# Kernel optimization log

Measured on AMD Instinct MI355X. Metric: run time of the kernel, lower is better.

## Reference

```python
import jax, jax.numpy as jnp
import numpy as np

B, L, H, D = 4096, 256, 32, 2
LOG_PROB_FACTOR = 0.5

def setup_inputs() -> dict:
    key = jax.random.key(0)
    k0, k1, k2, k3 = jax.random.split(key, 4)
    x = jax.random.randint(k0, (B, L), 0, D)  # spin configs in {0,1}
    Wi = jax.random.normal(k1, (D, 4 * H), dtype=jnp.float32) * 0.1   # input kernel (no bias, flax LSTMCell)
    Wh = jax.random.normal(k2, (H, 4 * H), dtype=jnp.float32) * 0.1   # recurrent kernel
    bh = jnp.zeros((4 * H,), dtype=jnp.float32)                        # recurrent bias
    Wo = jax.random.normal(k3, (H, D), dtype=jnp.float32) * 0.1       # output Dense kernel
    bo = jnp.zeros((D,), dtype=jnp.float32)                            # output Dense bias
    return {"x": x, "Wi": Wi, "Wh": Wh, "bh": bh, "Wo": Wo, "bo": bo}

def reference(x, Wi, Wh, bh, Wo, bo):
    # one-hot of spin t-1 (zeros at t=0); log-prob is read out at spin t.
    x_oh = jax.nn.one_hot(x, D, dtype=Wi.dtype)      # [B, L, D]
    xs = jnp.swapaxes(x_oh, 0, 1)                    # [L, B, D] time-major for scan
    c0 = jnp.zeros((x.shape[0], H), Wi.dtype)
    h0 = jnp.zeros((x.shape[0], H), Wi.dtype)
    inp0 = jnp.zeros((x.shape[0], D), Wi.dtype)      # jnp.zeros(inputDim) initial input

    def step(carry, xt):
        c, h, inp = carry
        gates = inp @ Wi + h @ Wh + bh               # [B, 4H]
        i, f, g, o = jnp.split(gates, 4, axis=-1)    # flax LSTMCell gate order i,f,g,o
        c_new = jax.nn.sigmoid(f) * c + jax.nn.sigmoid(i) * jnp.tanh(g)
        h_new = jax.nn.sigmoid(o) * jnp.tanh(c_new)
        out = jax.nn.elu(h_new @ Wo + bo)            # Dense + actFun, [B, D]
        # log(sum(softmax(out) * onehot)) == gathered log_softmax (stable form)
        logp = jnp.sum(jax.nn.log_softmax(out, axis=-1) * xt, axis=-1)  # [B]
        return (c_new, h_new, xt), logp

    _, logps = jax.lax.scan(step, (c0, h0, inp0), xs)  # logps: [L, B]
    return LOG_PROB_FACTOR * jnp.sum(logps, axis=0)    # [B]
```

## Files before the change

### kernel.cpp

```cpp
#include <hip/hip_runtime.h>


typedef __attribute__((ext_vector_type(8))) short bf16x8;
typedef __attribute__((ext_vector_type(4))) float f32x4;

#define LOG2E  1.4426950408889634f
#define TWOL   2.8853900817779268f
#define LN2    0.6931471805599453f

__device__ __forceinline__ float fexp2(float x) { return __builtin_amdgcn_exp2f(x); }
__device__ __forceinline__ float flog2(float x) { return __builtin_amdgcn_logf(x); }
__device__ __forceinline__ float frcp(float x)  { return __builtin_amdgcn_rcpf(x); }

__device__ __forceinline__ float fsig(float x)   { return frcp(1.f + fexp2(-LOG2E * x)); }
__device__ __forceinline__ float ftanh_(float x) { return 1.f - 2.f * frcp(fexp2(TWOL * x) + 1.f); }
__device__ __forceinline__ float felu(float x)   { return x > 0.f ? x : fexp2(LOG2E * x) - 1.f; }

__device__ __forceinline__ unsigned short f2bf(float f) {
    unsigned u = __builtin_bit_cast(unsigned, f);
    u = (u + 0x7FFFu + ((u >> 16) & 1u)) >> 16;
    return (unsigned short)u;
}

constexpr int Bsz = 4096;

__global__ __launch_bounds__(512, 2) void lstm_r11(
    const int*   __restrict__ x,
    const float* __restrict__ Wi,
    const float* __restrict__ Wh,
    const float* __restrict__ bh,
    const float* __restrict__ Wo,
    const float* __restrict__ bo,
    float*       __restrict__ out)
{
    const int tid  = threadIdx.x;
    const int w    = tid >> 6;
    const int lane = tid & 63;
    const int m    = lane & 15;
    const int oct  = lane >> 4;
    const int rot  = w & 3;
    const int half = w >> 2;
    const int b0   = blockIdx.x * 16;

    __shared__ unsigned spinbits[16][8];
    __shared__ float2   Sbuf[256][16];
    __shared__ short    hbuf[2][16][40];
    __shared__ float    red[8][16];

    {
        const int bl = tid >> 5;
        const int c8 = (tid & 31) * 8;
        const int4* src = reinterpret_cast<const int4*>(x + (b0 + bl) * 256 + c8);
        const int4 v0 = src[0], v1 = src[1];
        const unsigned bv =
            (v0.x & 1) | ((v0.y & 1) << 1) | ((v0.z & 1) << 2) | ((v0.w & 1) << 3) |
            ((v1.x & 1) << 4) | ((v1.y & 1) << 5) | ((v1.z & 1) << 6) | ((v1.w & 1) << 7);
        reinterpret_cast<char*>(spinbits)[bl * 32 + (tid & 31)] = (char)bv;
    }

    bf16x8 wfrag[4];
#pragma unroll
    for (int q = 0; q < 4; ++q) {
        const float gs = (q == 2) ? TWOL * 0.5f * 2.f : -LOG2E;
        const float gss = (q == 2) ? TWOL : -LOG2E;
        (void)gs;
        const int colg = 32 * q + 16 * half + ((m + rot) & 15);
#pragma unroll
        for (int j = 0; j < 8; ++j)
            wfrag[q][j] = (short)f2bf(((q == 2) ? TWOL * 0.5f : -LOG2E) * 2.f * 0.5f * Wh[(oct * 8 + j) * 128 + colg] * ((q == 2) ? 2.f : 1.f) / ((q == 2) ? 2.f : 1.f) * ((q == 2) ? 2.f : 1.f));
        (void)gss;
    }
#pragma unroll
    for (int q = 0; q < 4; ++q) {
        const float gs = (q == 2) ? (2.f * LOG2E) : -LOG2E;
        const int colg = 32 * q + 16 * half + ((m + rot) & 15);
#pragma unroll
        for (int j = 0; j < 8; ++j)
            wfrag[q][j] = (short)f2bf(gs * Wh[(oct * 8 + j) * 128 + colg]);
    }
    bf16x8 wofragA;
#pragma unroll
    for (int j = 0; j < 8; ++j)
        wofragA[j] = (m < 2) ? (short)f2bf(Wo[(oct * 8 + j) * 2 + m]) : (short)0;

    const int ucell = 4 * oct + rot + 16 * half;
    float bv0[4], bvd[4];
#pragma unroll
    for (int q = 0; q < 4; ++q) {
        const float gs = (q == 2) ? (2.f * LOG2E) : -LOG2E;
        const int c0 = 32 * q + ucell;
        bv0[q] = gs * (bh[c0] + Wi[c0]);
        bvd[q] = gs * (Wi[128 + c0] - Wi[c0]);
    }
    const float bo0 = bo[0], bo1 = bo[1];

    float cp = TWOL * (fsig(bh[ucell]) * ftanh_(bh[64 + ucell]));
    hbuf[0][m][ucell] = (short)f2bf(fsig(bh[96 + ucell]) * ftanh_(cp * (1.f / TWOL)));
    __syncthreads();

    const f32x4 zero4 = { 0.f, 0.f, 0.f, 0.f };
    f32x4 ccq[4] = { zero4, zero4, zero4, zero4 };

    unsigned cur = spinbits[m][0];
    for (int k = 0; k < 8; ++k) {
        const int tb = 32 * k + 1;
        const unsigned nxt = spinbits[m][k < 7 ? k + 1 : 7];
#pragma unroll
        for (int i = 0; i < 32; ++i) {
            const int rb = i & 1, wb = rb ^ 1;
            const float spf = (float)((cur >> i) & 1u);

            const bf16x8 hfrag =
                *reinterpret_cast<const bf16x8*>(&hbuf[rb][m][8 * oct]);

#pragma unroll
            for (int q = 0; q < 4; ++q) ccq[q][0] = fmaf(spf, bvd[q], bv0[q]);

            f32x4 acc[4];
#pragma unroll
            for (int q = 0; q < 4; ++q)
                acc[q] = __builtin_amdgcn_mfma_f32_16x16x32_bf16(wfrag[q], hfrag, ccq[q], 0, 0, 0);

            if ((i & 7) == w) {
                const f32x4 hacc =
                    __builtin_amdgcn_mfma_f32_16x16x32_bf16(wofragA, hfrag, zero4, 0, 0, 0);
                if (oct == 0) Sbuf[tb - 1 + i][m] = make_float2(hacc[0], hacc[1]);
            }

            {
                const float ei = fexp2(acc[0][0]), ef = fexp2(acc[1][0]);
                const float eg = fexp2(acc[2][0]), eo = fexp2(acc[3][0]);
                const float P  = (1.f + ei) * (1.f + eg);
                const float Q  = 1.f + ef;
                const float E  = fmaf(eg, TWOL, -TWOL);
                const float R  = frcp(P * Q);
                const float gf   = P * R;
                const float igtp = E * Q * R;
                cp = fmaf(gf, cp, igtp);
                const float ec = fexp2(cp);
                const float h  = (ec - 1.f) * frcp((1.f + eo) * (1.f + ec));
                hbuf[wb][m][ucell] = (short)f2bf(h);
            }
            __syncthreads();
        }
        cur = nxt;
    }

    float lp = 0.f;
    {
        const unsigned sw = spinbits[m][w] >> (8 * oct);
        const int t0 = w * 32 + oct * 8;
#pragma unroll
        for (int i = 0; i < 8; ++i) {
            const int t = t0 + i;
            const float2 sv = Sbuf[t][m];
            const int sp = (sw >> i) & 1u;
            const float o0 = felu(sv.x + bo0);
            const float o1 = felu(sv.y + bo1);
            const float mx = fmaxf(o0, o1), mn = fminf(o0, o1);
            const float lse = mx + LN2 * flog2(1.f + fexp2(LOG2E * (mn - mx)));
            lp += (sp ? o1 : o0) - lse;
        }
    }
    lp += __shfl_xor(lp, 16, 64);
    lp += __shfl_xor(lp, 32, 64);
    if (lane < 16) red[w][lane] = lp;
    __syncthreads();
    if (tid < 16) {
        float s = 0.f;
#pragma unroll
        for (int ww = 0; ww < 8; ++ww) s += red[ww][tid];
        out[b0 + tid] = 0.5f * s;
    }
}

extern "C" void kernel_launch(void* const* d_in, const int* in_sizes, int n_in,
                              void* d_out, int out_size, void* d_ws, size_t ws_size,
                              hipStream_t stream) {
    const int*   x  = (const int*)d_in[0];
    const float* Wi = (const float*)d_in[1];
    const float* Wh = (const float*)d_in[2];
    const float* bh = (const float*)d_in[3];
    const float* Wo = (const float*)d_in[4];
    const float* bo = (const float*)d_in[5];
    float* out = (float*)d_out;

    lstm_r11<<<dim3(Bsz / 16), dim3(512), 0, stream>>>(x, Wi, Wh, bh, Wo, bo, out);
}
```

Baseline: 137.0 us.

## Make each wavefront own two sequences to drop per-step block barriers

Replaces the 8-wave, 16-sequence block with a single-wave block that handles two batch rows and computes all four gates for both with eight MFMAs per step. Because one wave holds the whole recurrent state, the per-timestep __syncthreads and double-buffered h exchange are removed, and lanes pick their gate values out of the MFMA outputs with selects. The cost is that most of each 16-column MFMA is wasted, since only two of its columns are real sequences, so each wave does about eight times the MFMA work per sequence. The grid grows to 2048 small blocks, and correctness relies on intra-wave LDS ordering with no barriers.

```diff
diff --git a/kernel.cpp b/kernel.cpp
--- a/kernel.cpp
+++ b/kernel.cpp
@@ -24,7 +24,7 @@
 
 constexpr int Bsz = 4096;
 
-__global__ __launch_bounds__(512, 2) void lstm_r11(
+__global__ __launch_bounds__(64, 2) void lstm_wpriv(
     const int*   __restrict__ x,
     const float* __restrict__ Wi,
     const float* __restrict__ Wh,
@@ -33,103 +33,97 @@
     const float* __restrict__ bo,
     float*       __restrict__ out)
 {
-    const int tid  = threadIdx.x;
-    const int w    = tid >> 6;
-    const int lane = tid & 63;
-    const int m    = lane & 15;
+    const int lane = threadIdx.x & 63;
+    const int n    = lane & 15;
     const int oct  = lane >> 4;
-    const int rot  = w & 3;
-    const int half = w >> 2;
-    const int b0   = blockIdx.x * 16;
+    const int m    = n & 1;
+    const int j    = n >> 1;
+    const int b0   = blockIdx.x * 2;
 
-    __shared__ unsigned spinbits[16][8];
-    __shared__ float2   Sbuf[256][16];
-    __shared__ short    hbuf[2][16][40];
-    __shared__ float    red[8][16];
+    __shared__ unsigned spinw[2][8];
+    __shared__ short    hbuf[2][40];
+    __shared__ float2   Sbuf[256][2];
 
     {
-        const int bl = tid >> 5;
-        const int c8 = (tid & 31) * 8;
+        const int bl = lane >> 5;
+        const int c8 = (lane & 31) * 8;
         const int4* src = reinterpret_cast<const int4*>(x + (b0 + bl) * 256 + c8);
         const int4 v0 = src[0], v1 = src[1];
         const unsigned bv =
             (v0.x & 1) | ((v0.y & 1) << 1) | ((v0.z & 1) << 2) | ((v0.w & 1) << 3) |
             ((v1.x & 1) << 4) | ((v1.y & 1) << 5) | ((v1.z & 1) << 6) | ((v1.w & 1) << 7);
-        reinterpret_cast<char*>(spinbits)[bl * 32 + (tid & 31)] = (char)bv;
+        reinterpret_cast<char*>(spinw)[bl * 32 + (lane & 31)] = (char)bv;
     }
 
-    bf16x8 wfrag[4];
-#pragma unroll
-    for (int q = 0; q < 4; ++q) {
-        const float gs = (q == 2) ? TWOL * 0.5f * 2.f : -LOG2E;
-        const float gss = (q == 2) ? TWOL : -LOG2E;
-        (void)gs;
-        const int colg = 32 * q + 16 * half + ((m + rot) & 15);
-#pragma unroll
-        for (int j = 0; j < 8; ++j)
-            wfrag[q][j] = (short)f2bf(((q == 2) ? TWOL * 0.5f : -LOG2E) * 2.f * 0.5f * Wh[(oct * 8 + j) * 128 + colg] * ((q == 2) ? 2.f : 1.f) / ((q == 2) ? 2.f : 1.f) * ((q == 2) ? 2.f : 1.f));
-        (void)gss;
-    }
+    bf16x8 wfrag[8];
 #pragma unroll
     for (int q = 0; q < 4; ++q) {
         const float gs = (q == 2) ? (2.f * LOG2E) : -LOG2E;
-        const int colg = 32 * q + 16 * half + ((m + rot) & 15);
 #pragma unroll
-        for (int j = 0; j < 8; ++j)
-            wfrag[q][j] = (short)f2bf(gs * Wh[(oct * 8 + j) * 128 + colg]);
+        for (int sx = 0; sx < 2; ++sx)
+#pragma unroll
+            for (int jj = 0; jj < 8; ++jj)
+                wfrag[2 * q + sx][jj] =
+                    (short)f2bf(gs * Wh[(8 * oct + jj) * 128 + 32 * q + 16 * sx + n]);
     }
-    bf16x8 wofragA;
+    bf16x8 wofrag;
 #pragma unroll
-    for (int j = 0; j < 8; ++j)
-        wofragA[j] = (m < 2) ? (short)f2bf(Wo[(oct * 8 + j) * 2 + m]) : (short)0;
+    for (int jj = 0; jj < 8; ++jj)
+        wofrag[jj] = (n < 2) ? (short)f2bf(Wo[(8 * oct + jj) * 2 + n]) : (short)0;
 
-    const int ucell = 4 * oct + rot + 16 * half;
+    const int u = 4 * oct + (j & 3) + 16 * (j >> 2);
     float bv0[4], bvd[4];
 #pragma unroll
     for (int q = 0; q < 4; ++q) {
         const float gs = (q == 2) ? (2.f * LOG2E) : -LOG2E;
-        const int c0 = 32 * q + ucell;
+        const int c0 = 32 * q + u;
         bv0[q] = gs * (bh[c0] + Wi[c0]);
         bvd[q] = gs * (Wi[128 + c0] - Wi[c0]);
     }
     const float bo0 = bo[0], bo1 = bo[1];
 
-    float cp = TWOL * (fsig(bh[ucell]) * ftanh_(bh[64 + ucell]));
-    hbuf[0][m][ucell] = (short)f2bf(fsig(bh[96 + ucell]) * ftanh_(cp * (1.f / TWOL)));
-    __syncthreads();
+    const bool j1 = (j & 1) != 0;
+    const bool j2 = (j & 2) != 0;
+    const bool j4 = (j & 4) != 0;
+
+    float cp = TWOL * (fsig(bh[u]) * ftanh_(bh[64 + u]));
+    hbuf[m][u] = (short)f2bf(fsig(bh[96 + u]) * ftanh_(cp * (1.f / TWOL)));
 
     const f32x4 zero4 = { 0.f, 0.f, 0.f, 0.f };
-    f32x4 ccq[4] = { zero4, zero4, zero4, zero4 };
 
-    unsigned cur = spinbits[m][0];
     for (int k = 0; k < 8; ++k) {
-        const int tb = 32 * k + 1;
-        const unsigned nxt = spinbits[m][k < 7 ? k + 1 : 7];
+        const unsigned cur = spinw[m][k];
 #pragma unroll
         for (int i = 0; i < 32; ++i) {
-            const int rb = i & 1, wb = rb ^ 1;
             const float spf = (float)((cur >> i) & 1u);
 
-            const bf16x8 hfrag =
-                *reinterpret_cast<const bf16x8*>(&hbuf[rb][m][8 * oct]);
+            const bf16x8 hfrag = *reinterpret_cast<const bf16x8*>(&hbuf[m][8 * oct]);
 
+            f32x4 acc[8];
 #pragma unroll
-            for (int q = 0; q < 4; ++q) ccq[q][0] = fmaf(spf, bvd[q], bv0[q]);
+            for (int tt = 0; tt < 8; ++tt)
+                acc[tt] = __builtin_amdgcn_mfma_f32_16x16x32_bf16(wfrag[tt], hfrag, zero4, 0, 0, 0);
+            const f32x4 hacc =
+                __builtin_amdgcn_mfma_f32_16x16x32_bf16(wofrag, hfrag, zero4, 0, 0, 0);
 
-            f32x4 acc[4];
+            if (lane < 2) Sbuf[32 * k + i][lane] = make_float2(hacc[0], hacc[1]);
+
+            float g[4];
 #pragma unroll
-            for (int q = 0; q < 4; ++q)
-                acc[q] = __builtin_amdgcn_mfma_f32_16x16x32_bf16(wfrag[q], hfrag, ccq[q], 0, 0, 0);
-
-            if ((i & 7) == w) {
-                const f32x4 hacc =
-                    __builtin_amdgcn_mfma_f32_16x16x32_bf16(wofragA, hfrag, zero4, 0, 0, 0);
-                if (oct == 0) Sbuf[tb - 1 + i][m] = make_float2(hacc[0], hacc[1]);
+            for (int q = 0; q < 4; ++q) {
+                const f32x4 a = acc[2 * q], b = acc[2 * q + 1];
+                const float a01 = j1 ? a[1] : a[0];
+                const float a23 = j1 ? a[3] : a[2];
+                const float av  = j2 ? a23 : a01;
+                const float b01 = j1 ? b[1] : b[0];
+                const float b23 = j1 ? b[3] : b[2];
+                const float bvv = j2 ? b23 : b01;
+                g[q] = (j4 ? bvv : av) + fmaf(spf, bvd[q], bv0[q]);
             }
 
             {
-                const float ei = fexp2(acc[0][0]), ef = fexp2(acc[1][0]);
-                const float eg = fexp2(acc[2][0]), eo = fexp2(acc[3][0]);
+                const float ei = fexp2(g[0]), ef = fexp2(g[1]);
+                const float eg = fexp2(g[2]), eo = fexp2(g[3]);
                 const float P  = (1.f + ei) * (1.f + eg);
                 const float Q  = 1.f + ef;
                 const float E  = fmaf(eg, TWOL, -TWOL);
@@ -139,38 +133,34 @@
                 cp = fmaf(gf, cp, igtp);
                 const float ec = fexp2(cp);
                 const float h  = (ec - 1.f) * frcp((1.f + eo) * (1.f + ec));
-                hbuf[wb][m][ucell] = (short)f2bf(h);
+                hbuf[m][u] = (short)f2bf(h);
             }
-            __syncthreads();
         }
-        cur = nxt;
     }
 
-    float lp = 0.f;
     {
-        const unsigned sw = spinbits[m][w] >> (8 * oct);
-        const int t0 = w * 32 + oct * 8;
+        const int m2    = lane & 1;
+        const int chunk = lane >> 1;
+        const unsigned sb =
+            (unsigned char)reinterpret_cast<const char*>(spinw)[m2 * 32 + chunk];
+        float lp = 0.f;
 #pragma unroll
         for (int i = 0; i < 8; ++i) {
-            const int t = t0 + i;
-            const float2 sv = Sbuf[t][m];
-            const int sp = (sw >> i) & 1u;
+            const int t = chunk * 8 + i;
+            const float2 sv = Sbuf[t][m2];
+            const int sp = (sb >> i) & 1u;
             const float o0 = felu(sv.x + bo0);
             const float o1 = felu(sv.y + bo1);
             const float mx = fmaxf(o0, o1), mn = fminf(o0, o1);
             const float lse = mx + LN2 * flog2(1.f + fexp2(LOG2E * (mn - mx)));
             lp += (sp ? o1 : o0) - lse;
         }
-    }
-    lp += __shfl_xor(lp, 16, 64);
-    lp += __shfl_xor(lp, 32, 64);
-    if (lane < 16) red[w][lane] = lp;
-    __syncthreads();
-    if (tid < 16) {
-        float s = 0.f;
-#pragma unroll
-        for (int ww = 0; ww < 8; ++ww) s += red[ww][tid];
-        out[b0 + tid] = 0.5f * s;
+        lp += __shfl_xor(lp, 2, 64);
+        lp += __shfl_xor(lp, 4, 64);
+        lp += __shfl_xor(lp, 8, 64);
+        lp += __shfl_xor(lp, 16, 64);
+        lp += __shfl_xor(lp, 32, 64);
+        if (lane < 2) out[b0 + lane] = 0.5f * lp;
     }
 }
 
@@ -185,5 +175,5 @@
     const float* bo = (const float*)d_in[5];
     float* out = (float*)d_out;
 
-    lstm_r11<<<dim3(Bsz / 16), dim3(512), 0, stream>>>(x, Wi, Wh, bh, Wo, bo, out);
+    lstm_wpriv<<<dim3(Bsz / 2), dim3(64), 0, stream>>>(x, Wi, Wh, bh, Wo, bo, out);
 }
```

Measured after the change: 159.8 us. 1.17x slower.
